# Kernel optimization log

Measured on AMD Instinct MI355X. Metric: run time of the kernel, lower is better.

The kernel has to match this reference:

```python
import jax, jax.numpy as jnp
import numpy as np

BN_EPS = 1e-5

def setup_inputs() -> dict:
    key = jax.random.key(0)
    ks = jax.random.split(key, 6)
    N, C, T, V = 64, 64, 300, 25
    Ci, Co, S = 16, 64, 3  # inter_channels = out//4, num_subset = 3
    x = jax.random.normal(ks[0], (N, C, T, V), dtype=jnp.float32)
    # static (non-trainable) adjacency buffer; graph_attn is init.constant_(1)
    A_static = jax.random.uniform(ks[1], (S, V, V), dtype=jnp.float32)
    graph_attn = jnp.ones((S, V, V), jnp.float32)
    # stacked 1x1 conv weights for the 3 subsets: (S, out_c, in_c)
    Wg = jax.random.normal(ks[2], (S, Co, C), jnp.float32) * 0.05
    bg = jnp.zeros((S, Co), jnp.float32)
    Wa = jax.random.normal(ks[3], (S, Ci, C), jnp.float32) * 0.05
    ba = jnp.zeros((S, Ci), jnp.float32)
    Wb = jax.random.normal(ks[4], (S, Ci, C), jnp.float32) * 0.05
    bb = jnp.zeros((S, Ci), jnp.float32)
    # BatchNorm2d (eval mode: running stats)
    gamma = jnp.ones((Co,), jnp.float32)
    beta = jnp.zeros((Co,), jnp.float32)
    run_mean = jnp.zeros((Co,), jnp.float32)
    run_var = jnp.ones((Co,), jnp.float32)
    return {"x": x, "A_static": A_static, "graph_attn": graph_attn,
            "Wg": Wg, "bg": bg, "Wa": Wa, "ba": ba, "Wb": Wb, "bb": bb,
            "gamma": gamma, "beta": beta, "run_mean": run_mean, "run_var": run_var}

def _conv1x1(x, W, b):
    # x: (N,C,T,V), W: (O,C), b: (O,) -> (N,O,T,V)
    return jnp.einsum('nctv,oc->notv', x, W) + b[None, :, None, None]

def reference(x, A_static, graph_attn, Wg, bg, Wa, ba, Wb, bb, gamma, beta, run_mean, run_var):
    N, C, T, V = x.shape
    Ci = Wa.shape[1]
    A = A_static + graph_attn            # (3, V, V)
    x_flat = x.reshape(N, C * T, V)
    hidden = jnp.zeros((), x.dtype)
    for i in range(Wg.shape[0]):
        a = _conv1x1(x, Wa[i], ba[i])                                  # (N,Ci,T,V)
        b2 = _conv1x1(x, Wb[i], bb[i])                                 # (N,Ci,T,V)
        A1 = a.transpose(0, 3, 1, 2).reshape(N, V, Ci * T)             # (N,V,Ci*T)
        A2 = b2.reshape(N, Ci * T, V)                                  # (N,Ci*T,V)
        attn = jax.nn.softmax(jnp.matmul(A1, A2) / (Ci * T), axis=-2)  # softmax over dim -2
        attn = attn + A[i]                                             # (N,V,V)
        y = jnp.matmul(x_flat, attn).reshape(N, C, T, V)
        hidden = hidden + _conv1x1(y, Wg[i], bg[i])
    inv = (gamma / jnp.sqrt(run_var + BN_EPS))[None, :, None, None]
    hn = (hidden - run_mean[None, :, None, None]) * inv + beta[None, :, None, None]
    return jax.nn.relu(hn + x)  # in_channels == out_channels -> identity residual
```

## Files before the change

### kernel.cpp

```cpp
#include <hip/hip_runtime.h>

typedef unsigned short u16;
typedef __attribute__((ext_vector_type(8))) short short8;
typedef __attribute__((ext_vector_type(4))) unsigned short ushort4v;
typedef __attribute__((ext_vector_type(4))) float float4v;

#define NB 64
#define CB 64
#define TB 300
#define VB 25
#define TVB 7500
#define CTVB 480000

static __device__ __forceinline__ float bf2f(u16 a) {
    union { unsigned u; float f; } x; x.u = ((unsigned)a) << 16; return x.f;
}
static __device__ __forceinline__ u16 f2bf(float f) {
    union { float f; unsigned u; } x; x.f = f;
    unsigned r = x.u + 0x7fffu + ((x.u >> 16) & 1u);
    return (u16)(r >> 16);
}

__global__ __launch_bounds__(256) void kA(
    const float* __restrict__ xg, const float* __restrict__ Wa, const float* __restrict__ ba,
    const float* __restrict__ Wb, const float* __restrict__ bb, float* __restrict__ Sws)
{
    __shared__ u16 xT[4][32][72];
    __shared__ u16 asT[3][32][72];
    __shared__ u16 bsT[3][32][72];
    const int tid  = threadIdx.x;
    const int lane = tid & 63;
    const int w    = tid >> 6;
    const int l15  = lane & 15;
    const int q    = lane >> 4;
    const int n    = blockIdx.y;
    const int t0   = blockIdx.x * 20;

    for (int e = tid; e < 4 * 7 * 72; e += 256) {
        int tt = e / (7 * 72);
        int r  = e - tt * (7 * 72);
        xT[tt][25 + r / 72][r % 72] = 0;
    }

    short8 waf[2], wbf[2];
    float ba_r[4], bb_r[4];
    if (w < 3) {
        const float* wap = Wa + w * 1024;
        const float* wbp = Wb + w * 1024;
        #pragma unroll
        for (int kf = 0; kf < 2; ++kf) {
            short8 fa, fb;
            int base = l15 * 64 + kf * 32 + q * 8;
            #pragma unroll
            for (int j = 0; j < 8; ++j) {
                fa[j] = (short)f2bf(wap[base + j]);
                fb[j] = (short)f2bf(wbp[base + j]);
            }
            waf[kf] = fa; wbf[kf] = fb;
        }
        #pragma unroll
        for (int r = 0; r < 4; ++r) {
            ba_r[r] = ba[w * 16 + q * 4 + r];
            bb_r[r] = bb[w * 16 + q * 4 + r];
        }
    }

    float4v accS[3];
    #pragma unroll
    for (int i = 0; i < 3; ++i) accS[i] = (float4v){0.f, 0.f, 0.f, 0.f};

    const float* xb = xg + (size_t)n * CTVB;

    for (int g = 0; g < 5; ++g) {
        __syncthreads();
        for (int e = tid; e < 6400; e += 256) {
            int c = e / 100;
            int j = e - c * 100;
            int tt = j / 25;
            int u  = j - tt * 25;
            xT[tt][u][c] = f2bf(xb[c * TVB + (t0 + g * 4) * 25 + j]);
        }
        __syncthreads();
        if (w < 3) {
            #pragma unroll
            for (int tt = 0; tt < 4; ++tt) {
                float4v aA0 = {0,0,0,0}, aA1 = {0,0,0,0}, aB0 = {0,0,0,0}, aB1 = {0,0,0,0};
                #pragma unroll
                for (int kf = 0; kf < 2; ++kf) {
                    short8 x0 = *(const short8*)&xT[tt][l15][kf * 32 + q * 8];
                    short8 x1 = *(const short8*)&xT[tt][16 + l15][kf * 32 + q * 8];
                    aA0 = __builtin_amdgcn_mfma_f32_16x16x32_bf16(waf[kf], x0, aA0, 0, 0, 0);
                    aA1 = __builtin_amdgcn_mfma_f32_16x16x32_bf16(waf[kf], x1, aA1, 0, 0, 0);
                    aB0 = __builtin_amdgcn_mfma_f32_16x16x32_bf16(wbf[kf], x0, aB0, 0, 0, 0);
                    aB1 = __builtin_amdgcn_mfma_f32_16x16x32_bf16(wbf[kf], x1, aB1, 0, 0, 0);
                }
                ushort4v pa0, pa1, pb0, pb1;
                #pragma unroll
                for (int r = 0; r < 4; ++r) {
                    pa0[r] = f2bf(aA0[r] + ba_r[r]);
                    pa1[r] = f2bf(aA1[r] + ba_r[r]);
                    pb0[r] = f2bf(aB0[r] + bb_r[r]);
                    pb1[r] = f2bf(aB1[r] + bb_r[r]);
                }
                int kb = tt * 16 + q * 4;
                *(ushort4v*)&asT[w][l15][kb]      = pa0;
                *(ushort4v*)&asT[w][16 + l15][kb] = pa1;
                *(ushort4v*)&bsT[w][l15][kb]      = pb0;
                *(ushort4v*)&bsT[w][16 + l15][kb] = pb1;
            }
        }
        __syncthreads();
        const int mt = w >> 1, nt = w & 1;
        #pragma unroll
        for (int i = 0; i < 3; ++i) {
            #pragma unroll
            for (int ks = 0; ks < 2; ++ks) {
                short8 af  = *(const short8*)&asT[i][mt * 16 + l15][ks * 32 + q * 8];
                short8 bf_ = *(const short8*)&bsT[i][nt * 16 + l15][ks * 32 + q * 8];
                accS[i] = __builtin_amdgcn_mfma_f32_16x16x32_bf16(af, bf_, accS[i], 0, 0, 0);
            }
        }
    }
    const int mt = w >> 1, nt = w & 1;
    #pragma unroll
    for (int i = 0; i < 3; ++i) {
        #pragma unroll
        for (int r = 0; r < 4; ++r) {
            int u = mt * 16 + q * 4 + r;
            int v = nt * 16 + l15;
            if (u < 25 && v < 25)
                atomicAdd(&Sws[(i * 64 + n) * 625 + u * 25 + v], accS[i][r]);
        }
    }
}

__global__ __launch_bounds__(64) void kS(float* __restrict__ Sws,
    const float* __restrict__ Ast, const float* __restrict__ Gat)
{
    int g = blockIdx.x;
    int i = g >> 6;
    int v = threadIdx.x;
    if (v >= 25) return;
    float vals[25];
    float m = -1e30f;
    #pragma unroll
    for (int u = 0; u < 25; ++u) {
        float s = Sws[g * 625 + u * 25 + v] * (1.0f / 4800.0f);
        vals[u] = s;
        m = fmaxf(m, s);
    }
    float sum = 0.f;
    #pragma unroll
    for (int u = 0; u < 25; ++u) { float e = __expf(vals[u] - m); vals[u] = e; sum += e; }
    float isum = 1.f / sum;
    #pragma unroll
    for (int u = 0; u < 25; ++u) {
        int idx = i * 625 + u * 25 + v;
        Sws[g * 625 + u * 25 + v] = vals[u] * isum + Ast[idx] + Gat[idx];
    }
}

__global__ __launch_bounds__(256) void kB(
    const float* __restrict__ xg, const float* __restrict__ Wgp, const float* __restrict__ bgp,
    const float* __restrict__ gam, const float* __restrict__ bet, const float* __restrict__ rmu,
    const float* __restrict__ rva, const float* __restrict__ attnw, float* __restrict__ outg)
{
    __shared__ u16 xsu[6][64][32];
    __shared__ u16 ysT[32][200];
    __shared__ u16 pTs[3][32][40];
    const int tid  = threadIdx.x;
    const int lane = tid & 63;
    const int w    = tid >> 6;
    const int l15  = lane & 15;
    const int q    = lane >> 4;
    const int n    = blockIdx.y;
    const int t0   = blockIdx.x * 6;

    for (int e = tid; e < 3 * 32 * 40; e += 256) ((u16*)pTs)[e] = 0;
    const float* xb = xg + (size_t)n * CTVB;
    for (int e = tid; e < 64 * 150; e += 256) {
        int c = e / 150;
        int j = e - c * 150;
        int tt = j / 25;
        int u  = j - tt * 25;
        xsu[tt][c][u] = f2bf(xb[c * TVB + t0 * 25 + j]);
    }
    for (int e = tid; e < 6 * 64 * 7; e += 256) {
        int tt = e / (64 * 7);
        int r  = e - tt * (64 * 7);
        xsu[tt][r / 7][25 + r % 7] = 0;
    }
    __syncthreads();
    for (int e = tid; e < 1875; e += 256) {
        int i = e / 625;
        int r = e - i * 625;
        int u = r / 25;
        int v = r - u * 25;
        pTs[i][v][u] = f2bf(attnw[(i * 64 + n) * 625 + r]);
    }
    short8 wgf[6];
    const int o_row = w * 16 + l15;
    #pragma unroll
    for (int kf = 0; kf < 6; ++kf) {
        int i  = kf >> 1;
        int c0 = (kf & 1) * 32 + q * 8;
        const float* p = Wgp + i * 4096 + o_row * 64 + c0;
        short8 f;
        #pragma unroll
        for (int j = 0; j < 8; ++j) f[j] = (short)f2bf(p[j]);
        wgf[kf] = f;
    }
    float invr[4], add0r[4];
    #pragma unroll
    for (int r = 0; r < 4; ++r) {
        int o = w * 16 + q * 4 + r;
        float gv = gam[o], bt = bet[o], mu = rmu[o], vv = rva[o];
        float bgs = bgp[o] + bgp[64 + o] + bgp[128 + o];
        float iv = gv * rsqrtf(vv + 1e-5f);
        invr[r] = iv;
        add0r[r] = (bgs - mu) * iv + bt;
    }
    __syncthreads();
    short8 pf[3][2];
    #pragma unroll
    for (int i = 0; i < 3; ++i)
        #pragma unroll
        for (int nt = 0; nt < 2; ++nt)
            pf[i][nt] = *(const short8*)&pTs[i][nt * 16 + l15][q * 8];

    for (int tl = 0; tl < 6; ++tl) {
        short8 xf = *(const short8*)&xsu[tl][w * 16 + l15][q * 8];
        #pragma unroll
        for (int i = 0; i < 3; ++i) {
            #pragma unroll
            for (int nt = 0; nt < 2; ++nt) {
                float4v acc = {0, 0, 0, 0};
                acc = __builtin_amdgcn_mfma_f32_16x16x32_bf16(xf, pf[i][nt], acc, 0, 0, 0);
                ushort4v pk;
                #pragma unroll
                for (int r = 0; r < 4; ++r) pk[r] = f2bf(acc[r]);
                *(ushort4v*)&ysT[nt * 16 + l15][i * 64 + w * 16 + q * 4] = pk;
            }
        }
        __syncthreads();
        #pragma unroll
        for (int nt = 0; nt < 2; ++nt) {
            float4v acc = {0, 0, 0, 0};
            #pragma unroll
            for (int kf = 0; kf < 6; ++kf) {
                short8 yf = *(const short8*)&ysT[nt * 16 + l15][kf * 32 + q * 8];
                acc = __builtin_amdgcn_mfma_f32_16x16x32_bf16(wgf[kf], yf, acc, 0, 0, 0);
            }
            int v = nt * 16 + l15;
            if (v < 25) {
                size_t ob = (size_t)n * CTVB + (size_t)(t0 + tl) * 25 + v;
                #pragma unroll
                for (int r = 0; r < 4; ++r) {
                    int o = w * 16 + q * 4 + r;
                    float xres = bf2f(xsu[tl][o][v]);
                    float val = fmaf(acc[r], invr[r], add0r[r]) + xres;
                    val = fmaxf(val, 0.f);
                    outg[ob + (size_t)o * TVB] = val;
                }
            }
        }
        __syncthreads();
    }
}

extern "C" void kernel_launch(void* const* d_in, const int* in_sizes, int n_in,
                              void* d_out, int out_size, void* d_ws, size_t ws_size,
                              hipStream_t stream) {
    const float* x    = (const float*)d_in[0];
    const float* Ast  = (const float*)d_in[1];
    const float* Gat  = (const float*)d_in[2];
    const float* Wg   = (const float*)d_in[3];
    const float* bg   = (const float*)d_in[4];
    const float* Wa   = (const float*)d_in[5];
    const float* ba   = (const float*)d_in[6];
    const float* Wb   = (const float*)d_in[7];
    const float* bb   = (const float*)d_in[8];
    const float* gam  = (const float*)d_in[9];
    const float* bet  = (const float*)d_in[10];
    const float* rmu  = (const float*)d_in[11];
    const float* rva  = (const float*)d_in[12];
    float* out = (float*)d_out;
    float* Sws = (float*)d_ws;

    hipMemsetAsync(Sws, 0, 192 * 625 * sizeof(float), stream);
    kA<<<dim3(15, 64), 256, 0, stream>>>(x, Wa, ba, Wb, bb, Sws);
    kS<<<dim3(192), 64, 0, stream>>>(Sws, Ast, Gat);
    kB<<<dim3(50, 64), 256, 0, stream>>>(x, Wg, bg, gam, bet, rmu, rva, Sws, out);
}
```

Baseline: 364.8 us.

## Vectorize x loads, spread kA projection over all waves, retile kB to 4 timesteps

kA now loads x with float4 global reads and splits the 12 (timestep, subset) projection tasks across all four waves instead of leaving one wave idle. kB switches to 4 timesteps per block, giving 75 blocks per sample and float4-aligned loads. Occupancy hints are added to both launch bounds. The aim is better global load efficiency and better wave utilization. The cost is extra weight registers per wave in kA and padded shared layouts that may change bank conflicts.

```diff
diff --git a/kernel.cpp b/kernel.cpp
--- a/kernel.cpp
+++ b/kernel.cpp
@@ -5,10 +5,6 @@
 typedef __attribute__((ext_vector_type(4))) unsigned short ushort4v;
 typedef __attribute__((ext_vector_type(4))) float float4v;
 
-#define NB 64
-#define CB 64
-#define TB 300
-#define VB 25
 #define TVB 7500
 #define CTVB 480000
 
@@ -21,7 +17,7 @@
     return (u16)(r >> 16);
 }
 
-__global__ __launch_bounds__(256) void kA(
+__global__ __launch_bounds__(256, 3) void kA(
     const float* __restrict__ xg, const float* __restrict__ Wa, const float* __restrict__ ba,
     const float* __restrict__ Wb, const float* __restrict__ bb, float* __restrict__ Sws)
 {
@@ -42,11 +38,17 @@
         xT[tt][25 + r / 72][r % 72] = 0;
     }
 
-    short8 waf[2], wbf[2];
-    float ba_r[4], bb_r[4];
-    if (w < 3) {
-        const float* wap = Wa + w * 1024;
-        const float* wbp = Wb + w * 1024;
+    int tts[3], iis[3];
+    #pragma unroll
+    for (int m = 0; m < 3; ++m) { int u = w + 4 * m; tts[m] = u / 3; iis[m] = u - 3 * tts[m]; }
+
+    short8 waf[3][2], wbf[3][2];
+    float ba_r[3][4], bb_r[3][4];
+    #pragma unroll
+    for (int m = 0; m < 3; ++m) {
+        const int i = iis[m];
+        const float* wap = Wa + i * 1024;
+        const float* wbp = Wb + i * 1024;
         #pragma unroll
         for (int kf = 0; kf < 2; ++kf) {
             short8 fa, fb;
@@ -56,12 +58,12 @@
                 fa[j] = (short)f2bf(wap[base + j]);
                 fb[j] = (short)f2bf(wbp[base + j]);
             }
-            waf[kf] = fa; wbf[kf] = fb;
+            waf[m][kf] = fa; wbf[m][kf] = fb;
         }
         #pragma unroll
         for (int r = 0; r < 4; ++r) {
-            ba_r[r] = ba[w * 16 + q * 4 + r];
-            bb_r[r] = bb[w * 16 + q * 4 + r];
+            ba_r[m][r] = ba[i * 16 + q * 4 + r];
+            bb_r[m][r] = bb[i * 16 + q * 4 + r];
         }
     }
 
@@ -73,41 +75,46 @@
 
     for (int g = 0; g < 5; ++g) {
         __syncthreads();
-        for (int e = tid; e < 6400; e += 256) {
-            int c = e / 100;
-            int j = e - c * 100;
-            int tt = j / 25;
-            int u  = j - tt * 25;
-            xT[tt][u][c] = f2bf(xb[c * TVB + (t0 + g * 4) * 25 + j]);
-        }
-        __syncthreads();
-        if (w < 3) {
-            #pragma unroll
-            for (int tt = 0; tt < 4; ++tt) {
-                float4v aA0 = {0,0,0,0}, aA1 = {0,0,0,0}, aB0 = {0,0,0,0}, aB1 = {0,0,0,0};
-                #pragma unroll
-                for (int kf = 0; kf < 2; ++kf) {
-                    short8 x0 = *(const short8*)&xT[tt][l15][kf * 32 + q * 8];
-                    short8 x1 = *(const short8*)&xT[tt][16 + l15][kf * 32 + q * 8];
-                    aA0 = __builtin_amdgcn_mfma_f32_16x16x32_bf16(waf[kf], x0, aA0, 0, 0, 0);
-                    aA1 = __builtin_amdgcn_mfma_f32_16x16x32_bf16(waf[kf], x1, aA1, 0, 0, 0);
-                    aB0 = __builtin_amdgcn_mfma_f32_16x16x32_bf16(wbf[kf], x0, aB0, 0, 0, 0);
-                    aB1 = __builtin_amdgcn_mfma_f32_16x16x32_bf16(wbf[kf], x1, aB1, 0, 0, 0);
-                }
-                ushort4v pa0, pa1, pb0, pb1;
-                #pragma unroll
-                for (int r = 0; r < 4; ++r) {
-                    pa0[r] = f2bf(aA0[r] + ba_r[r]);
-                    pa1[r] = f2bf(aA1[r] + ba_r[r]);
-                    pb0[r] = f2bf(aB0[r] + bb_r[r]);
-                    pb1[r] = f2bf(aB1[r] + bb_r[r]);
-                }
-                int kb = tt * 16 + q * 4;
-                *(ushort4v*)&asT[w][l15][kb]      = pa0;
-                *(ushort4v*)&asT[w][16 + l15][kb] = pa1;
-                *(ushort4v*)&bsT[w][l15][kb]      = pb0;
-                *(ushort4v*)&bsT[w][16 + l15][kb] = pb1;
-            }
+        for (int e = tid; e < 1600; e += 256) {
+            int c = e / 25;
+            int j = e - c * 25;
+            float4v xv = *(const float4v*)(xb + (size_t)c * TVB + (t0 + g * 4) * 25 + j * 4);
+            #pragma unroll
+            for (int k2 = 0; k2 < 4; ++k2) {
+                int idx = j * 4 + k2;
+                int tt = idx / 25;
+                int uu = idx - tt * 25;
+                xT[tt][uu][c] = f2bf(xv[k2]);
+            }
+        }
+        __syncthreads();
+        #pragma unroll
+        for (int m = 0; m < 3; ++m) {
+            const int tt = tts[m];
+            const int i  = iis[m];
+            float4v aA0 = {0,0,0,0}, aA1 = {0,0,0,0}, aB0 = {0,0,0,0}, aB1 = {0,0,0,0};
+            #pragma unroll
+            for (int kf = 0; kf < 2; ++kf) {
+                short8 x0 = *(const short8*)&xT[tt][l15][kf * 32 + q * 8];
+                short8 x1 = *(const short8*)&xT[tt][16 + l15][kf * 32 + q * 8];
+                aA0 = __builtin_amdgcn_mfma_f32_16x16x32_bf16(waf[m][kf], x0, aA0, 0, 0, 0);
+                aA1 = __builtin_amdgcn_mfma_f32_16x16x32_bf16(waf[m][kf], x1, aA1, 0, 0, 0);
+                aB0 = __builtin_amdgcn_mfma_f32_16x16x32_bf16(wbf[m][kf], x0, aB0, 0, 0, 0);
+                aB1 = __builtin_amdgcn_mfma_f32_16x16x32_bf16(wbf[m][kf], x1, aB1, 0, 0, 0);
+            }
+            ushort4v pa0, pa1, pb0, pb1;
+            #pragma unroll
+            for (int r = 0; r < 4; ++r) {
+                pa0[r] = f2bf(aA0[r] + ba_r[m][r]);
+                pa1[r] = f2bf(aA1[r] + ba_r[m][r]);
+                pb0[r] = f2bf(aB0[r] + bb_r[m][r]);
+                pb1[r] = f2bf(aB1[r] + bb_r[m][r]);
+            }
+            int kb = tt * 16 + q * 4;
+            *(ushort4v*)&asT[i][l15][kb]      = pa0;
+            *(ushort4v*)&asT[i][16 + l15][kb] = pa1;
+            *(ushort4v*)&bsT[i][l15][kb]      = pb0;
+            *(ushort4v*)&bsT[i][16 + l15][kb] = pb1;
         }
         __syncthreads();
         const int mt = w >> 1, nt = w & 1;
@@ -160,32 +167,37 @@
     }
 }
 
-__global__ __launch_bounds__(256) void kB(
+__global__ __launch_bounds__(256, 4) void kB(
     const float* __restrict__ xg, const float* __restrict__ Wgp, const float* __restrict__ bgp,
     const float* __restrict__ gam, const float* __restrict__ bet, const float* __restrict__ rmu,
     const float* __restrict__ rva, const float* __restrict__ attnw, float* __restrict__ outg)
 {
-    __shared__ u16 xsu[6][64][32];
+    __shared__ u16 xsu[4][64][40];
     __shared__ u16 ysT[32][200];
-    __shared__ u16 pTs[3][32][40];
+    __shared__ u16 pTs[3][32][32];
     const int tid  = threadIdx.x;
     const int lane = tid & 63;
     const int w    = tid >> 6;
     const int l15  = lane & 15;
     const int q    = lane >> 4;
     const int n    = blockIdx.y;
-    const int t0   = blockIdx.x * 6;
-
-    for (int e = tid; e < 3 * 32 * 40; e += 256) ((u16*)pTs)[e] = 0;
+    const int t0   = blockIdx.x * 4;
+
+    for (int e = tid; e < 3 * 32 * 32; e += 256) ((u16*)pTs)[e] = 0;
     const float* xb = xg + (size_t)n * CTVB;
-    for (int e = tid; e < 64 * 150; e += 256) {
-        int c = e / 150;
-        int j = e - c * 150;
-        int tt = j / 25;
-        int u  = j - tt * 25;
-        xsu[tt][c][u] = f2bf(xb[c * TVB + t0 * 25 + j]);
-    }
-    for (int e = tid; e < 6 * 64 * 7; e += 256) {
+    for (int e = tid; e < 1600; e += 256) {
+        int c = e / 25;
+        int j = e - c * 25;
+        float4v xv = *(const float4v*)(xb + (size_t)c * TVB + t0 * 25 + j * 4);
+        #pragma unroll
+        for (int k = 0; k < 4; ++k) {
+            int idx = j * 4 + k;
+            int tt = idx / 25;
+            int u  = idx - tt * 25;
+            xsu[tt][c][u] = f2bf(xv[k]);
+        }
+    }
+    for (int e = tid; e < 4 * 64 * 7; e += 256) {
         int tt = e / (64 * 7);
         int r  = e - tt * (64 * 7);
         xsu[tt][r / 7][25 + r % 7] = 0;
@@ -228,7 +240,7 @@
         for (int nt = 0; nt < 2; ++nt)
             pf[i][nt] = *(const short8*)&pTs[i][nt * 16 + l15][q * 8];
 
-    for (int tl = 0; tl < 6; ++tl) {
+    for (int tl = 0; tl < 4; ++tl) {
         short8 xf = *(const short8*)&xsu[tl][w * 16 + l15][q * 8];
         #pragma unroll
         for (int i = 0; i < 3; ++i) {
@@ -290,5 +302,5 @@
     hipMemsetAsync(Sws, 0, 192 * 625 * sizeof(float), stream);
     kA<<<dim3(15, 64), 256, 0, stream>>>(x, Wa, ba, Wb, bb, Sws);
     kS<<<dim3(192), 64, 0, stream>>>(Sws, Ast, Gat);
-    kB<<<dim3(50, 64), 256, 0, stream>>>(x, Wg, bg, gam, bet, rmu, rva, Sws, out);
-}
+    kB<<<dim3(75, 64), 256, 0, stream>>>(x, Wg, bg, gam, bet, rmu, rva, Sws, out);
+}
```

After: 361.0 us. No clear change (-1.0%).
